# Kernel optimization log

Hardware: AMD Instinct MI355X
Metric: run time of the kernel (lower is better)

Reference implementation:

```python
import jax, jax.numpy as jnp
import numpy as np

B, T, D, N, H = 1, 256, 512, 8, 64  # batch, seq, d_model, n_heads, d_head
INIT_STD = 0.02
IGNORE = -1000000.0
DUMMY_LOGIT = -1000.0


def setup_inputs() -> dict:
    key = jax.random.key(0)
    ks = jax.random.split(key, 9)
    std = INIT_STD
    inp = {
        'normalized_resid_pre': jax.random.normal(ks[0], (B, T, D), dtype=jnp.float32),
        'W_K1': jax.random.normal(ks[1], (N, D, H), dtype=jnp.float32) * std,
        'W_K2': jax.random.normal(ks[2], (N, D, H), dtype=jnp.float32) * std,
        'W_Q':  jax.random.normal(ks[3], (N, D, H), dtype=jnp.float32) * std,
        'W_V1': jax.random.normal(ks[4], (N, D, H), dtype=jnp.float32) * std,
        'W_V2': jax.random.normal(ks[5], (N, D, H), dtype=jnp.float32) * std,
        'W_Kq': jax.random.normal(ks[6], (N, H, H, H), dtype=jnp.float32) * std,
        'W_Vq': jax.random.normal(ks[7], (N, H, H, H), dtype=jnp.float32) * std,
        'W_O':  jax.random.normal(ks[8], (N, H, D), dtype=jnp.float32) * std,
        'b_K1': jnp.zeros((N, H), dtype=jnp.float32),
        'b_K2': jnp.zeros((N, H), dtype=jnp.float32),
        'b_Q':  jnp.zeros((N, H), dtype=jnp.float32),
        'b_V1': jnp.zeros((N, H), dtype=jnp.float32),
        'b_V2': jnp.zeros((N, H), dtype=jnp.float32),
        'b_O':  jnp.zeros((D,), dtype=jnp.float32),
    }
    return inp


def _trittention(x, W_K1, W_K2, W_Q, W_V1, W_V2, W_Kq, W_Vq, W_O,
                 b_K1, b_K2, b_Q, b_V1, b_V2, b_O):
    b, t, d = x.shape
    n, _, h = W_Q.shape
    proj = lambda W, bias: jnp.einsum('ndh,bpd->bpnh', W, x) + bias
    k1 = proj(W_K1, b_K1)  # (b, t, n, h)
    k2 = proj(W_K2, b_K2)
    q  = proj(W_Q,  b_Q)
    v1 = proj(W_V1, b_V1)
    v2 = proj(W_V2, b_V2)

    # bilinear value over pairs of positions: (b, n, h, s, t) -> flatten (s t)
    v = jnp.einsum('bsni,btnj,nijh->bnhst', v1, v2, W_Vq)
    v = v.reshape(b, n, h, t * t)

    # cubic scores: (b, n, s, t, r) with s=k1 pos, t=k2 pos, r=query pos
    step1 = jnp.einsum('brnk,nijk->bnrij', q, W_Kq)
    step2 = jnp.einsum('bnrij,btnj->bnrit', step1, k2)
    attn = jnp.einsum('bnrit,bsni->bnstr', step2, k1)

    # causal + ordering mask (order_attn=True, attn_eq=False):
    # masked if s>=r or t>=r or s>=t
    s_idx = jnp.arange(t)[:, None, None]
    t_idx = jnp.arange(t)[None, :, None]
    r_idx = jnp.arange(t)[None, None, :]
    mask = (s_idx >= r_idx) | (t_idx >= r_idx) | (s_idx >= t_idx)
    attn = jnp.where(mask, IGNORE, attn)

    # rearrange 'b n s t r -> b n r (s t)' and scale by d_head
    attn = jnp.transpose(attn, (0, 1, 4, 2, 3)).reshape(b, n, t, t * t) / h

    # causal_attn=True: append dummy logit / zero value slot
    dummy_logit = jnp.full((b, n, t, 1), DUMMY_LOGIT, dtype=attn.dtype)
    attn = jnp.concatenate([attn, dummy_logit], axis=-1)
    dummy_value = jnp.zeros((b, n, h, 1), dtype=v.dtype)
    v = jnp.concatenate([v, dummy_value], axis=-1)

    attn = jax.nn.softmax(attn, axis=-1)
    z = jnp.einsum('bnql,bnhl->bqnh', attn, v)
    out = jnp.einsum('bpnh,nhd->bpd', z, W_O) + b_O  # sum over heads folded in
    return out


def reference(normalized_resid_pre, W_K1, W_K2, W_Q, W_V1, W_V2, W_Kq, W_Vq, W_O,
              b_K1, b_K2, b_Q, b_V1, b_V2, b_O):
    return _trittention(normalized_resid_pre, W_K1, W_K2, W_Q, W_V1, W_V2,
                        W_Kq, W_Vq, W_O, b_K1, b_K2, b_Q, b_V1, b_V2, b_O)
```

## Files before the change

kernel.cpp:

```cpp
#include <hip/hip_runtime.h>
#include <hip/hip_bf16.h>
#include <math.h>

#define TT 256
#define DD 512
#define NN 8
#define HH 64
#define PROJ 131072

typedef __attribute__((ext_vector_type(8))) short short8v;
typedef __attribute__((ext_vector_type(4))) short short4v;
typedef __attribute__((ext_vector_type(4))) float f32x4;

__device__ __forceinline__ short f2bf(float x) {
    union { float f; unsigned u; } v; v.f = x;
    unsigned r = (v.u + 0x7FFFu + ((v.u >> 16) & 1u)) >> 16;
    return (short)r;
}

#define LGKM0 asm volatile("s_waitcnt lgkmcnt(0)" ::: "memory")

#define F_NUM  0
#define F_DEN  131072
#define F_END  133120
#define S_PB   0
#define S_XB   655360
#define S_WB   786432
#define S_KQB  2097152
#define S_VQB  4194304
#define S_WOB  6291456
#define S_S1B  6553600
#define S_AB   14942208
#define S_GB   23330816

__global__ __launch_bounds__(256) void prep_kernel(
    const float* __restrict__ x, const float* __restrict__ W_Kq,
    const float* __restrict__ W0, const float* __restrict__ W1,
    const float* __restrict__ W2, const float* __restrict__ W3,
    const float* __restrict__ W4, const float* __restrict__ Vq,
    const float* __restrict__ WO, short* __restrict__ sb, float* __restrict__ fz)
{
    __shared__ float plds[64 * 129];
    int b = blockIdx.x;
    int tid = threadIdx.x;
    if (b < 1024) {
        int i = b * 256 + tid;
        const float4 f0 = *(const float4*)(W_Kq + (size_t)i * 8);
        const float4 f1 = *(const float4*)(W_Kq + (size_t)i * 8 + 4);
        short8v o;
        o[0]=f2bf(f0.x); o[1]=f2bf(f0.y); o[2]=f2bf(f0.z); o[3]=f2bf(f0.w);
        o[4]=f2bf(f1.x); o[5]=f2bf(f1.y); o[6]=f2bf(f1.z); o[7]=f2bf(f1.w);
        *(short8v*)(sb + S_KQB + (size_t)i * 8) = o;
    } else if (b < 1088) {
        int i = (b - 1024) * 256 + tid;
        const float4 f0 = *(const float4*)(x + (size_t)i * 8);
        const float4 f1 = *(const float4*)(x + (size_t)i * 8 + 4);
        short8v o;
        o[0]=f2bf(f0.x); o[1]=f2bf(f0.y); o[2]=f2bf(f0.z); o[3]=f2bf(f0.w);
        o[4]=f2bf(f1.x); o[5]=f2bf(f1.y); o[6]=f2bf(f1.z); o[7]=f2bf(f1.w);
        *(short8v*)(sb + S_XB + (size_t)i * 8) = o;
    } else if (b < 1128) {
        int pn = b - 1088; int p = pn >> 3, n = pn & 7;
        const float* Wp = (p==0)?W0:(p==1)?W1:(p==2)?W2:(p==3)?W3:W4;
        const float* src = Wp + (size_t)n * DD * HH;
        short* dst = sb + S_WB + (size_t)pn * HH * DD;
        for (int d0 = 0; d0 < DD; d0 += 64) {
            __syncthreads();
            for (int it = 0; it < 16; ++it) {
                int m = it * 256 + tid;
                int dl = m >> 6, h = m & 63;
                plds[h * 65 + dl] = src[(size_t)(d0 + dl) * 64 + h];
            }
            __syncthreads();
            int h = tid >> 2, seg = tid & 3;
            short8v o0, o1;
            #pragma unroll
            for (int e = 0; e < 8; ++e) o0[e] = f2bf(plds[h * 65 + seg * 16 + e]);
            #pragma unroll
            for (int e = 0; e < 8; ++e) o1[e] = f2bf(plds[h * 65 + seg * 16 + 8 + e]);
            *(short8v*)(dst + (size_t)h * DD + d0 + seg * 16) = o0;
            *(short8v*)(dst + (size_t)h * DD + d0 + seg * 16 + 8) = o1;
        }
    } else if (b < 1640) {
        int bb = b - 1128; int n = bb >> 6, i = bb & 63;
        const float* src = Vq + (size_t)(n * 64 + i) * 4096;
        for (int it = 0; it < 16; ++it) {
            int m = it * 256 + tid;
            int j = m >> 6, h = m & 63;
            plds[h * 65 + j] = src[(size_t)j * 64 + h];
        }
        __syncthreads();
        int h = tid >> 2, seg = tid & 3;
        short8v o0, o1;
        #pragma unroll
        for (int e = 0; e < 8; ++e) o0[e] = f2bf(plds[h * 65 + seg * 16 + e]);
        #pragma unroll
        for (int e = 0; e < 8; ++e) o1[e] = f2bf(plds[h * 65 + seg * 16 + 8 + e]);
        short* dst = sb + S_VQB + (size_t)n * 262144 + (size_t)h * 4096 + i * 64 + seg * 16;
        *(short8v*)dst = o0;
        *(short8v*)(dst + 8) = o1;
    } else if (b < 1672) {
        int bb = b - 1640; int dc = bb & 7, nhc = bb >> 3;
        for (int it = 0; it < 32; ++it) {
            int m = it * 256 + tid;
            int nhl = m >> 6, dl = m & 63;
            plds[dl * 129 + nhl] = WO[(size_t)(nhc * 128 + nhl) * 512 + dc * 64 + dl];
        }
        __syncthreads();
        for (int it = 0; it < 4; ++it) {
            int m = it * 256 + tid;
            int dl = m >> 4, seg = m & 15;
            short8v o;
            #pragma unroll
            for (int e = 0; e < 8; ++e) o[e] = f2bf(plds[dl * 129 + seg * 8 + e]);
            *(short8v*)(sb + S_WOB + (size_t)(dc * 64 + dl) * 512 + nhc * 128 + seg * 8) = o;
        }
    } else {
        int i = (b - 1672) * 1024 + tid * 4;
        *(float4*)(fz + i) = make_float4(0.f, 0.f, 0.f, 0.f);
    }
}

__global__ __launch_bounds__(512) void proj_kernel(
    const short* __restrict__ xb, const short* __restrict__ Wb,
    const float* __restrict__ bK1, const float* __restrict__ bK2,
    const float* __restrict__ bQ,  const float* __restrict__ bV1,
    const float* __restrict__ bV2, short* __restrict__ Pb) {
    int p = blockIdx.x, n = blockIdx.y, mhalf = blockIdx.z;
    int wv = threadIdx.x >> 6, lane = threadIdx.x & 63, g = lane >> 4, c = lane & 15;
    __shared__ short wlds[64 * 520];
    __shared__ short sbuf[8][16 * 72];
    const short* wsrc = Wb + (size_t)(p * 8 + n) * HH * DD;
    for (int it = 0; it < 8; ++it) {
        int idx = it * 512 + threadIdx.x;
        int h = idx >> 6, seg = idx & 63;
        *(short8v*)(&wlds[h * 520 + seg * 8]) = *(const short8v*)(wsrc + (size_t)h * DD + seg * 8);
    }
    __syncthreads();
    int mt = mhalf * 8 + wv;
    f32x4 acc[4];
    #pragma unroll
    for (int ct = 0; ct < 4; ++ct) acc[ct] = (f32x4){0.f, 0.f, 0.f, 0.f};
    for (int ks = 0; ks < 16; ++ks) {
        short8v a = *(const short8v*)(xb + (size_t)(mt * 16 + c) * DD + ks * 32 + g * 8);
        #pragma unroll
        for (int ct = 0; ct < 4; ++ct) {
            short8v b = *(const short8v*)(&wlds[(ct * 16 + c) * 520 + ks * 32 + g * 8]);
            acc[ct] = __builtin_amdgcn_mfma_f32_16x16x32_bf16(a, b, acc[ct], 0, 0, 0);
        }
    }
    const float* bp = (p == 0) ? bK1 : (p == 1) ? bK2 : (p == 2) ? bQ : (p == 3) ? bV1 : bV2;
    short* sbw = &sbuf[wv][0];
    #pragma unroll
    for (int ct = 0; ct < 4; ++ct) {
        float bias = bp[n * 64 + ct * 16 + c];
        #pragma unroll
        for (int m = 0; m < 4; ++m)
            sbw[(g * 4 + m) * 72 + ct * 16 + c] = f2bf(acc[ct][m] + bias);
    }
    LGKM0;
    int rl = lane & 15, sg = lane >> 4;
    short8v o0 = *(const short8v*)(&sbw[rl * 72 + sg * 16]);
    short8v o1 = *(const short8v*)(&sbw[rl * 72 + sg * 16 + 8]);
    short* dst = Pb + (size_t)p * PROJ + (size_t)(n * 256 + mt * 16 + rl) * 64 + sg * 16;
    *(short8v*)dst = o0;
    *(short8v*)(dst + 8) = o1;
}

__global__ __launch_bounds__(256) void bgemm_kernel(
    const short* __restrict__ A0, const short* __restrict__ B0, short* __restrict__ O0,
    const short* __restrict__ A1, const short* __restrict__ B1, short* __restrict__ O1) {
    int mt = blockIdx.x, n = blockIdx.y, z = blockIdx.z;
    const short* A = (z < 4) ? A0 : A1;
    const short* B = (z < 4) ? B0 : B1;
    short* out = (z < 4) ? O0 : O1;
    int cgq = z & 3;
    int wv = threadIdx.x >> 6, lane = threadIdx.x & 63, g = lane >> 4, c = lane & 15;
    __shared__ short sbuf[4][16 * 72];
    short* sbw = &sbuf[wv][0];
    const short* abase = A + ((size_t)n * 256 + mt * 16 + c) * 64 + g * 8;
    short8v a0 = *(const short8v*)abase;
    short8v a1 = *(const short8v*)(abase + 32);
    for (int cg = cgq * 16 + wv; cg < cgq * 16 + 16; cg += 4) {
        f32x4 acc[4];
        #pragma unroll
        for (int jt = 0; jt < 4; ++jt) acc[jt] = (f32x4){0.f, 0.f, 0.f, 0.f};
        const short* bb = B + ((size_t)n * 4096 + cg * 64) * 64;
        #pragma unroll
        for (int jt = 0; jt < 4; ++jt) {
            short8v b0 = *(const short8v*)(bb + (size_t)(jt * 16 + c) * 64 + g * 8);
            short8v b1 = *(const short8v*)(bb + (size_t)(jt * 16 + c) * 64 + g * 8 + 32);
            acc[jt] = __builtin_amdgcn_mfma_f32_16x16x32_bf16(a0, b0, acc[jt], 0, 0, 0);
            acc[jt] = __builtin_amdgcn_mfma_f32_16x16x32_bf16(a1, b1, acc[jt], 0, 0, 0);
        }
        LGKM0;
        #pragma unroll
        for (int jt = 0; jt < 4; ++jt)
            #pragma unroll
            for (int m = 0; m < 4; ++m)
                sbw[(g * 4 + m) * 72 + jt * 16 + c] = f2bf(acc[jt][m]);
        LGKM0;
        int rl = lane & 15, sg = lane >> 4;
        short8v o0 = *(const short8v*)(&sbw[rl * 72 + sg * 16]);
        short8v o1 = *(const short8v*)(&sbw[rl * 72 + sg * 16 + 8]);
        short* dst = out + ((size_t)n * 256 + mt * 16 + rl) * 4096 + cg * 64 + sg * 16;
        *(short8v*)dst = o0;
        *(short8v*)(dst + 8) = o1;
    }
}

__global__ __launch_bounds__(256) void gmat_kernel(const short* __restrict__ S1b,
                                                   const short* __restrict__ K2b,
                                                   short* __restrict__ G) {
    int bid = blockIdx.x;
    int n = bid & 7;
    int tt = (bid >> 3) & 15;
    int rq = bid >> 7;
    int wv = threadIdx.x >> 6, lane = threadIdx.x & 63, g = lane >> 4, c = lane & 15;
    int t0 = tt * 16;
    __shared__ short sbuf[4][16 * 68];
    short* sbw = &sbuf[wv][0];
    const short* abase = K2b + ((size_t)n * TT + t0 + c) * 64 + g * 8;
    short8v a0 = *(const short8v*)abase;
    short8v a1 = *(const short8v*)(abase + 32);
    for (int r = t0 + rq * 4 + wv; r < 256; r += 16) {
        const short* bb = S1b + ((size_t)(n * 256 + r) * 64) * 64;
        f32x4 acc[4];
        #pragma unroll
        for (int it = 0; it < 4; ++it) {
            short8v b0 = *(const short8v*)(bb + (size_t)(it * 16 + c) * 64 + g * 8);
            short8v b1 = *(const short8v*)(bb + (size_t)(it * 16 + c) * 64 + g * 8 + 32);
            acc[it] = (f32x4){0.f, 0.f, 0.f, 0.f};
            acc[it] = __builtin_amdgcn_mfma_f32_16x16x32_bf16(a0, b0, acc[it], 0, 0, 0);
            acc[it] = __builtin_amdgcn_mfma_f32_16x16x32_bf16(a1, b1, acc[it], 0, 0, 0);
        }
        LGKM0;
        #pragma unroll
        for (int it = 0; it < 4; ++it)
            #pragma unroll
            for (int m = 0; m < 4; ++m)
                sbw[(g * 4 + m) * 68 + it * 16 + c] = f2bf(acc[it][m]);
        LGKM0;
        int trow = lane >> 2, seg = (lane & 3) * 16;
        short8v o0 = *(const short8v*)(&sbw[trow * 68 + seg]);
        short8v o1 = *(const short8v*)(&sbw[trow * 68 + seg + 8]);
        short* dst = G + (((size_t)(n * TT + t0 + trow)) * TT + r) * 64 + seg;
        *(short8v*)dst = o0;
        *(short8v*)(dst + 8) = o1;
    }
}

__global__ __launch_bounds__(1024) void attn_kernel(
    const short* __restrict__ K1b, const short* __restrict__ V1b,
    const short* __restrict__ Gm, const short* __restrict__ Ab,
    float* __restrict__ num, float* __restrict__ den)
{
    int bid = blockIdx.x;
    int n = bid & 7;
    int rest = bid >> 3;
    int pair = rest >> 2;
    int sig = rest & 3;
    int tid = threadIdx.x;
    int wv = tid >> 6, lane = tid & 63, g = lane >> 4, c = lane & 15;

    __shared__ short k1lds[64 * 72];
    __shared__ short v1lds[64 * 72];
    __shared__ short u_lds[8][64][68];

    int t0H = (31 - pair) * 8;
    int stmaxK = (t0H + 6) >> 4;
    int cntK = (stmaxK >= sig) ? ((stmaxK - sig) >> 2) + 1 : 0;
    for (int idx = tid; idx < cntK * 128; idx += 1024) {
        int row = idx >> 3, seg = idx & 7;
        int s = (sig + (row >> 4) * 4) * 16 + (row & 15);
        *(short8v*)(&k1lds[row * 72 + seg * 8]) =
            *(const short8v*)(K1b + ((size_t)n * TT + s) * 64 + seg * 8);
        *(short8v*)(&v1lds[row * 72 + seg * 8]) =
            *(const short8v*)(V1b + ((size_t)n * TT + s) * 64 + seg * 8);
    }
    __syncthreads();

    f32x4 numacc[4];
    #pragma unroll
    for (int b = 0; b < 4; ++b) numacc[b] = (f32x4){0.f, 0.f, 0.f, 0.f};
    float denacc = 0.f;
    int rt = wv;
    int lU = wv >> 2, hU = wv & 3;

    const short* vr = &v1lds[(lU * 16 + c) * 72 + g * 8];
    short8v vf0 = *(const short8v*)vr;
    short8v vf1 = *(const short8v*)(vr + 32);

    for (int part = 0; part < 2; ++part) {
        int t0 = part ? t0H : pair * 8;

        __syncthreads();
        for (int tl = 0; tl < 8; ++tl) {
            int t = t0 + tl;
            int stm = (t - 1) >> 4;
            int cntU = (t >= 1 && stm >= sig) ? ((stm - sig) >> 2) + 1 : 0;
            if (lU >= cntU) continue;
            const short* ar = Ab + (size_t)(n * TT + t) * 4096 + (hU * 16 + c) * 64 + g * 8;
            short8v ab0 = *(const short8v*)ar;
            short8v ab1 = *(const short8v*)(ar + 32);
            f32x4 ucc = (f32x4){0.f, 0.f, 0.f, 0.f};
            ucc = __builtin_amdgcn_mfma_f32_16x16x32_bf16(vf0, ab0, ucc, 0, 0, 0);
            ucc = __builtin_amdgcn_mfma_f32_16x16x32_bf16(vf1, ab1, ucc, 0, 0, 0);
            short4v uo;
            #pragma unroll
            for (int m = 0; m < 4; ++m) uo[m] = f2bf(ucc[m]);
            *(short4v*)(&u_lds[tl][hU * 16 + c][lU * 16 + g * 4]) = uo;
        }
        __syncthreads();

        for (int tl = 0; tl < 8; ++tl) {
            int t = t0 + tl;
            if (t < 1 || t > 254) continue;
            int rt_start = (t + 1) >> 4;
            int stmaxU = (t - 1) >> 4;
            int cntU = (stmaxU >= sig) ? ((stmaxU - sig) >> 2) + 1 : 0;
            if (cntU == 0 || rt < rt_start) continue;

            const short* gb = Gm + (((size_t)(n * TT + t) * TT) + rt * 16 + c) * 64 + g * 8;
            short8v gf0 = *(const short8v*)gb;
            short8v gf1 = *(const short8v*)(gb + 32);
            int r = rt * 16 + c;

            for (int loc = 0; loc < cntU; ++loc) {
                int s_base = (sig + loc * 4) * 16;
                const short* kr = &k1lds[(loc * 16 + c) * 72 + g * 8];
                short8v af0 = *(const short8v*)kr;
                short8v af1 = *(const short8v*)(kr + 32);
                f32x4 lg = (f32x4){0.f, 0.f, 0.f, 0.f};
                lg = __builtin_amdgcn_mfma_f32_16x16x32_bf16(af0, gf0, lg, 0, 0, 0);
                lg = __builtin_amdgcn_mfma_f32_16x16x32_bf16(af1, gf1, lg, 0, 0, 0);
                short4v eb;
                float dsum = 0.f;
                #pragma unroll
                for (int m = 0; m < 4; ++m) {
                    int s = s_base + g * 4 + m;
                    float e = (s < t && r > t) ? __expf(lg[m] * 0.015625f) : 0.f;
                    dsum += e;
                    eb[m] = f2bf(e);
                }
                denacc += dsum;
                #pragma unroll
                for (int hs = 0; hs < 4; ++hs) {
                    short4v ub = *(const short4v*)(&u_lds[tl][hs * 16 + c][loc * 16 + g * 4]);
                    numacc[hs] = __builtin_amdgcn_mfma_f32_16x16x16bf16_1k(eb, ub, numacc[hs], 0, 0, 0);
                }
            }
        }
    }

    if (__any(denacc != 0.f)) {
        float v = denacc;
        v += __shfl_xor(v, 16);
        v += __shfl_xor(v, 32);
        if (lane < 16) atomicAdd(&den[n * TT + rt * 16 + lane], v);
        #pragma unroll
        for (int hs = 0; hs < 4; ++hs)
            #pragma unroll
            for (int m = 0; m < 4; ++m)
                atomicAdd(&num[((size_t)(n * TT + rt * 16 + g * 4 + m)) * 64 + hs * 16 + c],
                          numacc[hs][m]);
    }
}

__global__ __launch_bounds__(512) void out_kernel(const float* __restrict__ num,
                                                  const float* __restrict__ den,
                                                  const short* __restrict__ WOb,
                                                  const float* __restrict__ bO,
                                                  float* __restrict__ out) {
    int mt = blockIdx.x & 15, dq = blockIdx.x >> 4;
    int wv = threadIdx.x >> 6, lane = threadIdx.x & 63, g = lane >> 4, c = lane & 15;
    int dt0 = dq * 16 + wv * 2;
    int t = mt * 16 + c;
    f32x4 acc[2];
    acc[0] = (f32x4){0.f, 0.f, 0.f, 0.f};
    acc[1] = (f32x4){0.f, 0.f, 0.f, 0.f};
    for (int ks = 0; ks < 16; ++ks) {
        int nh = ks * 32 + g * 8;
        int nn = nh >> 6, h = nh & 63;
        float dv = den[nn * 256 + t];
        float rcp = (dv > 0.f) ? 1.f / dv : 0.f;
        const float* np = num + ((size_t)(nn * 256 + t) * 64 + h);
        float4 f0 = *(const float4*)np;
        float4 f1 = *(const float4*)(np + 4);
        short8v a;
        a[0]=f2bf(f0.x*rcp); a[1]=f2bf(f0.y*rcp); a[2]=f2bf(f0.z*rcp); a[3]=f2bf(f0.w*rcp);
        a[4]=f2bf(f1.x*rcp); a[5]=f2bf(f1.y*rcp); a[6]=f2bf(f1.z*rcp); a[7]=f2bf(f1.w*rcp);
        #pragma unroll
        for (int u = 0; u < 2; ++u) {
            short8v b = *(const short8v*)(WOb + (size_t)((dt0 + u) * 16 + c) * 512 + ks * 32 + g * 8);
            acc[u] = __builtin_amdgcn_mfma_f32_16x16x32_bf16(a, b, acc[u], 0, 0, 0);
        }
    }
    #pragma unroll
    for (int u = 0; u < 2; ++u) {
        int d = (dt0 + u) * 16 + c;
        float bias = bO[d];
        #pragma unroll
        for (int m = 0; m < 4; ++m)
            out[(size_t)(mt * 16 + g * 4 + m) * 512 + d] = acc[u][m] + bias;
    }
}

extern "C" void kernel_launch(void* const* d_in, const int* in_sizes, int n_in,
                              void* d_out, int out_size, void* d_ws, size_t ws_size,
                              hipStream_t stream) {
    const float* x    = (const float*)d_in[0];
    const float* W_K1 = (const float*)d_in[1];
    const float* W_K2 = (const float*)d_in[2];
    const float* W_Q  = (const float*)d_in[3];
    const float* W_V1 = (const float*)d_in[4];
    const float* W_V2 = (const float*)d_in[5];
    const float* W_Kq = (const float*)d_in[6];
    const float* W_Vq = (const float*)d_in[7];
    const float* W_O  = (const float*)d_in[8];
    const float* b_K1 = (const float*)d_in[9];
    const float* b_K2 = (const float*)d_in[10];
    const float* b_Q  = (const float*)d_in[11];
    const float* b_V1 = (const float*)d_in[12];
    const float* b_V2 = (const float*)d_in[13];
    const float* b_O  = (const float*)d_in[14];
    float* ws = (float*)d_ws;
    short* sb = (short*)(ws + F_END);
    float* out = (float*)d_out;

    prep_kernel<<<1802, 256, 0, stream>>>(x, W_Kq, W_K1, W_K2, W_Q, W_V1, W_V2,
                                          W_Vq, W_O, sb, ws + F_NUM);

    proj_kernel<<<dim3(5, 8, 2), 512, 0, stream>>>(sb + S_XB, sb + S_WB,
                                                   b_K1, b_K2, b_Q, b_V1, b_V2, sb + S_PB);

    bgemm_kernel<<<dim3(16, 8, 8), 256, 0, stream>>>(
        sb + S_PB + 2 * PROJ, sb + S_KQB, sb + S_S1B,
        sb + S_PB + 4 * PROJ, sb + S_VQB, sb + S_AB);

    gmat_kernel<<<512, 256, 0, stream>>>(sb + S_S1B, sb + S_PB + 1 * PROJ, sb + S_GB);

    attn_kernel<<<512, 1024, 0, stream>>>(sb + S_PB, sb + S_PB + 3 * PROJ,
                                          sb + S_GB, sb + S_AB,
                                          ws + F_NUM, ws + F_DEN);

    out_kernel<<<32, 512, 0, stream>>>(ws + F_NUM, ws + F_DEN, sb + S_WOB, b_O, out);
}
```

Measured before the change: 152.3 us.

## Re-split attention work into smaller blocks with double-buffered U tiles

Attention work is re-partitioned. Blocks shrink from 1024 to 512 threads and each covers one 8-position t-chunk and one half of the query row tiles, replacing the old pairing of a low and a high t-chunk; the grid grows from 512 to 1536 blocks. The per-t U tile is now computed inline into a two-slot LDS buffer with one barrier per t instead of an 8-slot staging pass, which cuts LDS use so more blocks fit per CU. Blocks with no work exit early. The trade-offs are recomputing the K1/V1 loads and U per half-split, plus possible load imbalance because the old triangular pairing is gone.

```diff
diff --git a/kernel.cpp b/kernel.cpp
--- a/kernel.cpp
+++ b/kernel.cpp
@@ -250,27 +250,31 @@
     }
 }
 
-__global__ __launch_bounds__(1024) void attn_kernel(
+__global__ __launch_bounds__(512, 8) void attn_kernel(
     const short* __restrict__ K1b, const short* __restrict__ V1b,
     const short* __restrict__ Gm, const short* __restrict__ Ab,
     float* __restrict__ num, float* __restrict__ den)
 {
     int bid = blockIdx.x;
     int n = bid & 7;
-    int rest = bid >> 3;
-    int pair = rest >> 2;
-    int sig = rest & 3;
+    int sig = (bid >> 3) & 3;
+    int q = bid >> 5;
+    int tc, rthalf;
+    if (q < 32) { tc = q >> 1; rthalf = q & 1; }
+    else        { tc = q - 16; rthalf = 1; }
     int tid = threadIdx.x;
     int wv = tid >> 6, lane = tid & 63, g = lane >> 4, c = lane & 15;
 
+    int t0 = tc * 8;
+    int stmaxK = (t0 + 6) >> 4;
+    int cntK = (stmaxK >= sig) ? ((stmaxK - sig) >> 2) + 1 : 0;
+    if (cntK == 0) return;
+
     __shared__ short k1lds[64 * 72];
     __shared__ short v1lds[64 * 72];
-    __shared__ short u_lds[8][64][68];
-
-    int t0H = (31 - pair) * 8;
-    int stmaxK = (t0H + 6) >> 4;
-    int cntK = (stmaxK >= sig) ? ((stmaxK - sig) >> 2) + 1 : 0;
-    for (int idx = tid; idx < cntK * 128; idx += 1024) {
+    __shared__ short u_lds[2][64][68];
+
+    for (int idx = tid; idx < cntK * 128; idx += 512) {
         int row = idx >> 3, seg = idx & 7;
         int s = (sig + (row >> 4) * 4) * 16 + (row & 15);
         *(short8v*)(&k1lds[row * 72 + seg * 8]) =
@@ -280,47 +284,59 @@
     }
     __syncthreads();
 
+    int hU = wv & 3, locA = wv >> 2, locB = locA + 2;
+    int rt = rthalf * 8 + wv;
+    int rtmax = rthalf * 8 + 7;
+
     f32x4 numacc[4];
     #pragma unroll
     for (int b = 0; b < 4; ++b) numacc[b] = (f32x4){0.f, 0.f, 0.f, 0.f};
     float denacc = 0.f;
-    int rt = wv;
-    int lU = wv >> 2, hU = wv & 3;
-
-    const short* vr = &v1lds[(lU * 16 + c) * 72 + g * 8];
-    short8v vf0 = *(const short8v*)vr;
-    short8v vf1 = *(const short8v*)(vr + 32);
-
-    for (int part = 0; part < 2; ++part) {
-        int t0 = part ? t0H : pair * 8;
-
-        __syncthreads();
-        for (int tl = 0; tl < 8; ++tl) {
-            int t = t0 + tl;
-            int stm = (t - 1) >> 4;
-            int cntU = (t >= 1 && stm >= sig) ? ((stm - sig) >> 2) + 1 : 0;
-            if (lU >= cntU) continue;
+    int ub = 0;
+
+    for (int tl = 0; tl < 8; ++tl) {
+        int t = t0 + tl;
+        if (t < 1 || t > 254) continue;
+        int stmaxU = (t - 1) >> 4;
+        int cntU = (stmaxU >= sig) ? ((stmaxU - sig) >> 2) + 1 : 0;
+        if (cntU == 0) continue;
+        int rt_start = (t + 1) >> 4;
+        if (rt_start > rtmax) continue;
+
+        short (*uw)[68] = u_lds[ub]; ub ^= 1;
+        int nT = cntU * 4;
+        if (wv < nT) {
             const short* ar = Ab + (size_t)(n * TT + t) * 4096 + (hU * 16 + c) * 64 + g * 8;
             short8v ab0 = *(const short8v*)ar;
             short8v ab1 = *(const short8v*)(ar + 32);
-            f32x4 ucc = (f32x4){0.f, 0.f, 0.f, 0.f};
-            ucc = __builtin_amdgcn_mfma_f32_16x16x32_bf16(vf0, ab0, ucc, 0, 0, 0);
-            ucc = __builtin_amdgcn_mfma_f32_16x16x32_bf16(vf1, ab1, ucc, 0, 0, 0);
-            short4v uo;
-            #pragma unroll
-            for (int m = 0; m < 4; ++m) uo[m] = f2bf(ucc[m]);
-            *(short4v*)(&u_lds[tl][hU * 16 + c][lU * 16 + g * 4]) = uo;
+            {
+                const short* vr = &v1lds[(locA * 16 + c) * 72 + g * 8];
+                short8v vf0 = *(const short8v*)vr;
+                short8v vf1 = *(const short8v*)(vr + 32);
+                f32x4 u = (f32x4){0.f, 0.f, 0.f, 0.f};
+                u = __builtin_amdgcn_mfma_f32_16x16x32_bf16(vf0, ab0, u, 0, 0, 0);
+                u = __builtin_amdgcn_mfma_f32_16x16x32_bf16(vf1, ab1, u, 0, 0, 0);
+                short4v uo;
+                #pragma unroll
+                for (int m = 0; m < 4; ++m) uo[m] = f2bf(u[m]);
+                *(short4v*)(&uw[hU * 16 + c][locA * 16 + g * 4]) = uo;
+            }
+            if (wv + 8 < nT) {
+                const short* vr = &v1lds[(locB * 16 + c) * 72 + g * 8];
+                short8v vf0 = *(const short8v*)vr;
+                short8v vf1 = *(const short8v*)(vr + 32);
+                f32x4 u = (f32x4){0.f, 0.f, 0.f, 0.f};
+                u = __builtin_amdgcn_mfma_f32_16x16x32_bf16(vf0, ab0, u, 0, 0, 0);
+                u = __builtin_amdgcn_mfma_f32_16x16x32_bf16(vf1, ab1, u, 0, 0, 0);
+                short4v uo;
+                #pragma unroll
+                for (int m = 0; m < 4; ++m) uo[m] = f2bf(u[m]);
+                *(short4v*)(&uw[hU * 16 + c][locB * 16 + g * 4]) = uo;
+            }
         }
         __syncthreads();
 
-        for (int tl = 0; tl < 8; ++tl) {
-            int t = t0 + tl;
-            if (t < 1 || t > 254) continue;
-            int rt_start = (t + 1) >> 4;
-            int stmaxU = (t - 1) >> 4;
-            int cntU = (stmaxU >= sig) ? ((stmaxU - sig) >> 2) + 1 : 0;
-            if (cntU == 0 || rt < rt_start) continue;
-
+        if (rt >= rt_start) {
             const short* gb = Gm + (((size_t)(n * TT + t) * TT) + rt * 16 + c) * 64 + g * 8;
             short8v gf0 = *(const short8v*)gb;
             short8v gf1 = *(const short8v*)(gb + 32);
@@ -346,8 +362,8 @@
                 denacc += dsum;
                 #pragma unroll
                 for (int hs = 0; hs < 4; ++hs) {
-                    short4v ub = *(const short4v*)(&u_lds[tl][hs * 16 + c][loc * 16 + g * 4]);
-                    numacc[hs] = __builtin_amdgcn_mfma_f32_16x16x16bf16_1k(eb, ub, numacc[hs], 0, 0, 0);
+                    short4v ubf = *(const short4v*)(&uw[hs * 16 + c][loc * 16 + g * 4]);
+                    numacc[hs] = __builtin_amdgcn_mfma_f32_16x16x16bf16_1k(eb, ubf, numacc[hs], 0, 0, 0);
                 }
             }
         }
@@ -440,7 +456,7 @@
 
     gmat_kernel<<<512, 256, 0, stream>>>(sb + S_S1B, sb + S_PB + 1 * PROJ, sb + S_GB);
 
-    attn_kernel<<<512, 1024, 0, stream>>>(sb + S_PB, sb + S_PB + 3 * PROJ,
+    attn_kernel<<<1536, 512, 0, stream>>>(sb + S_PB, sb + S_PB + 3 * PROJ,
                                           sb + S_GB, sb + S_AB,
                                           ws + F_NUM, ws + F_DEN);
 
```

Result: no change. 151.1 us (-0.8%).

## Reassociate trilinear scores via K2·W_Kq and drop the G-matrix kernel

Applied to the files above, without the earlier changes.

The cubic score contraction is reassociated. bgemm now multiplies K2 by a transposed W_Kq to build a per-t matrix M. attn_kernel computes Y = M·q on the fly per query tile, then contracts it with K1, instead of reading a precomputed G tensor of size (t, r, i) from memory. This removes the gmat_kernel and its large global write and read. It also regrids attn_kernel into 768 blocks of 512 threads over (t chunk, r half), with per-t U tiles built in shared memory. The cost is extra MFMA work to recompute Y per t, and the new work split may be less balanced.

```diff
diff --git a/kernel.cpp b/kernel.cpp
--- a/kernel.cpp
+++ b/kernel.cpp
@@ -29,9 +29,8 @@
 #define S_KQB  2097152
 #define S_VQB  4194304
 #define S_WOB  6291456
-#define S_S1B  6553600
+#define S_MB   6553600
 #define S_AB   14942208
-#define S_GB   23330816
 
 __global__ __launch_bounds__(256) void prep_kernel(
     const float* __restrict__ x, const float* __restrict__ W_Kq,
@@ -43,24 +42,34 @@
     __shared__ float plds[64 * 129];
     int b = blockIdx.x;
     int tid = threadIdx.x;
-    if (b < 1024) {
-        int i = b * 256 + tid;
-        const float4 f0 = *(const float4*)(W_Kq + (size_t)i * 8);
-        const float4 f1 = *(const float4*)(W_Kq + (size_t)i * 8 + 4);
-        short8v o;
-        o[0]=f2bf(f0.x); o[1]=f2bf(f0.y); o[2]=f2bf(f0.z); o[3]=f2bf(f0.w);
-        o[4]=f2bf(f1.x); o[5]=f2bf(f1.y); o[6]=f2bf(f1.z); o[7]=f2bf(f1.w);
-        *(short8v*)(sb + S_KQB + (size_t)i * 8) = o;
-    } else if (b < 1088) {
-        int i = (b - 1024) * 256 + tid;
+    if (b < 512) {
+        int n = b >> 6, i = b & 63;
+        const float* src = W_Kq + (size_t)(n * 64 + i) * 4096;
+        for (int it = 0; it < 16; ++it) {
+            int m = it * 256 + tid;
+            int j = m >> 6, k = m & 63;
+            plds[k * 65 + j] = src[m];
+        }
+        __syncthreads();
+        int k = tid >> 2, seg = tid & 3;
+        short8v o0, o1;
+        #pragma unroll
+        for (int e = 0; e < 8; ++e) o0[e] = f2bf(plds[k * 65 + seg * 16 + e]);
+        #pragma unroll
+        for (int e = 0; e < 8; ++e) o1[e] = f2bf(plds[k * 65 + seg * 16 + 8 + e]);
+        short* dst = sb + S_KQB + (size_t)n * 262144 + (size_t)(i * 64 + k) * 64 + seg * 16;
+        *(short8v*)dst = o0;
+        *(short8v*)(dst + 8) = o1;
+    } else if (b < 576) {
+        int i = (b - 512) * 256 + tid;
         const float4 f0 = *(const float4*)(x + (size_t)i * 8);
         const float4 f1 = *(const float4*)(x + (size_t)i * 8 + 4);
         short8v o;
         o[0]=f2bf(f0.x); o[1]=f2bf(f0.y); o[2]=f2bf(f0.z); o[3]=f2bf(f0.w);
         o[4]=f2bf(f1.x); o[5]=f2bf(f1.y); o[6]=f2bf(f1.z); o[7]=f2bf(f1.w);
         *(short8v*)(sb + S_XB + (size_t)i * 8) = o;
-    } else if (b < 1128) {
-        int pn = b - 1088; int p = pn >> 3, n = pn & 7;
+    } else if (b < 616) {
+        int pn = b - 576; int p = pn >> 3, n = pn & 7;
         const float* Wp = (p==0)?W0:(p==1)?W1:(p==2)?W2:(p==3)?W3:W4;
         const float* src = Wp + (size_t)n * DD * HH;
         short* dst = sb + S_WB + (size_t)pn * HH * DD;
@@ -81,8 +90,8 @@
             *(short8v*)(dst + (size_t)h * DD + d0 + seg * 16) = o0;
             *(short8v*)(dst + (size_t)h * DD + d0 + seg * 16 + 8) = o1;
         }
-    } else if (b < 1640) {
-        int bb = b - 1128; int n = bb >> 6, i = bb & 63;
+    } else if (b < 1128) {
+        int bb = b - 616; int n = bb >> 6, i = bb & 63;
         const float* src = Vq + (size_t)(n * 64 + i) * 4096;
         for (int it = 0; it < 16; ++it) {
             int m = it * 256 + tid;
@@ -99,8 +108,8 @@
         short* dst = sb + S_VQB + (size_t)n * 262144 + (size_t)h * 4096 + i * 64 + seg * 16;
         *(short8v*)dst = o0;
         *(short8v*)(dst + 8) = o1;
-    } else if (b < 1672) {
-        int bb = b - 1640; int dc = bb & 7, nhc = bb >> 3;
+    } else if (b < 1160) {
+        int bb = b - 1128; int dc = bb & 7, nhc = bb >> 3;
         for (int it = 0; it < 32; ++it) {
             int m = it * 256 + tid;
             int nhl = m >> 6, dl = m & 63;
@@ -116,7 +125,7 @@
             *(short8v*)(sb + S_WOB + (size_t)(dc * 64 + dl) * 512 + nhc * 128 + seg * 8) = o;
         }
     } else {
-        int i = (b - 1672) * 1024 + tid * 4;
+        int i = (b - 1160) * 1024 + tid * 4;
         *(float4*)(fz + i) = make_float4(0.f, 0.f, 0.f, 0.f);
     }
 }
@@ -209,146 +218,104 @@
     }
 }
 
-__global__ __launch_bounds__(256) void gmat_kernel(const short* __restrict__ S1b,
-                                                   const short* __restrict__ K2b,
-                                                   short* __restrict__ G) {
-    int bid = blockIdx.x;
-    int n = bid & 7;
-    int tt = (bid >> 3) & 15;
-    int rq = bid >> 7;
-    int wv = threadIdx.x >> 6, lane = threadIdx.x & 63, g = lane >> 4, c = lane & 15;
-    int t0 = tt * 16;
-    __shared__ short sbuf[4][16 * 68];
-    short* sbw = &sbuf[wv][0];
-    const short* abase = K2b + ((size_t)n * TT + t0 + c) * 64 + g * 8;
-    short8v a0 = *(const short8v*)abase;
-    short8v a1 = *(const short8v*)(abase + 32);
-    for (int r = t0 + rq * 4 + wv; r < 256; r += 16) {
-        const short* bb = S1b + ((size_t)(n * 256 + r) * 64) * 64;
-        f32x4 acc[4];
-        #pragma unroll
-        for (int it = 0; it < 4; ++it) {
-            short8v b0 = *(const short8v*)(bb + (size_t)(it * 16 + c) * 64 + g * 8);
-            short8v b1 = *(const short8v*)(bb + (size_t)(it * 16 + c) * 64 + g * 8 + 32);
-            acc[it] = (f32x4){0.f, 0.f, 0.f, 0.f};
-            acc[it] = __builtin_amdgcn_mfma_f32_16x16x32_bf16(a0, b0, acc[it], 0, 0, 0);
-            acc[it] = __builtin_amdgcn_mfma_f32_16x16x32_bf16(a1, b1, acc[it], 0, 0, 0);
-        }
-        LGKM0;
-        #pragma unroll
-        for (int it = 0; it < 4; ++it)
-            #pragma unroll
-            for (int m = 0; m < 4; ++m)
-                sbw[(g * 4 + m) * 68 + it * 16 + c] = f2bf(acc[it][m]);
-        LGKM0;
-        int trow = lane >> 2, seg = (lane & 3) * 16;
-        short8v o0 = *(const short8v*)(&sbw[trow * 68 + seg]);
-        short8v o1 = *(const short8v*)(&sbw[trow * 68 + seg + 8]);
-        short* dst = G + (((size_t)(n * TT + t0 + trow)) * TT + r) * 64 + seg;
-        *(short8v*)dst = o0;
-        *(short8v*)(dst + 8) = o1;
-    }
-}
-
-__global__ __launch_bounds__(1024) void attn_kernel(
+__global__ __launch_bounds__(512, 6) void attn_kernel(
     const short* __restrict__ K1b, const short* __restrict__ V1b,
-    const short* __restrict__ Gm, const short* __restrict__ Ab,
+    const short* __restrict__ Qb,  const short* __restrict__ Mb,
+    const short* __restrict__ Ab,
     float* __restrict__ num, float* __restrict__ den)
 {
     int bid = blockIdx.x;
     int n = bid & 7;
-    int rest = bid >> 3;
-    int pair = rest >> 2;
-    int sig = rest & 3;
+    int z = bid >> 3;
+    int tc4, rthalf;
+    if (z < 64) { tc4 = z >> 1; rthalf = z & 1; }
+    else        { tc4 = z - 32; rthalf = 1; }
     int tid = threadIdx.x;
     int wv = tid >> 6, lane = tid & 63, g = lane >> 4, c = lane & 15;
-
-    __shared__ short k1lds[64 * 72];
-    __shared__ short v1lds[64 * 72];
-    __shared__ short u_lds[8][64][68];
-
-    int t0H = (31 - pair) * 8;
-    int stmaxK = (t0H + 6) >> 4;
-    int cntK = (stmaxK >= sig) ? ((stmaxK - sig) >> 2) + 1 : 0;
-    for (int idx = tid; idx < cntK * 128; idx += 1024) {
-        int row = idx >> 3, seg = idx & 7;
-        int s = (sig + (row >> 4) * 4) * 16 + (row & 15);
-        *(short8v*)(&k1lds[row * 72 + seg * 8]) =
-            *(const short8v*)(K1b + ((size_t)n * TT + s) * 64 + seg * 8);
-        *(short8v*)(&v1lds[row * 72 + seg * 8]) =
-            *(const short8v*)(V1b + ((size_t)n * TT + s) * 64 + seg * 8);
-    }
-    __syncthreads();
+    int rt = rthalf * 8 + wv;
+    int t0 = tc4 * 4;
+
+    __shared__ short u_lds[64 * 260];
+    __shared__ short mlds[64 * 72];
+
+    const short* qrow = Qb + ((size_t)(n * 256) + rt * 16 + c) * 64 + g * 8;
+    short8v qf0 = *(const short8v*)qrow;
+    short8v qf1 = *(const short8v*)(qrow + 32);
 
     f32x4 numacc[4];
     #pragma unroll
     for (int b = 0; b < 4; ++b) numacc[b] = (f32x4){0.f, 0.f, 0.f, 0.f};
     float denacc = 0.f;
-    int rt = wv;
-    int lU = wv >> 2, hU = wv & 3;
-
-    const short* vr = &v1lds[(lU * 16 + c) * 72 + g * 8];
-    short8v vf0 = *(const short8v*)vr;
-    short8v vf1 = *(const short8v*)(vr + 32);
-
-    for (int part = 0; part < 2; ++part) {
-        int t0 = part ? t0H : pair * 8;
+
+    for (int tl = 0; tl < 4; ++tl) {
+        int t = t0 + tl;
+        int cntU = (t >= 1 && t <= 254) ? (((t - 1) >> 4) + 1) : 0;
 
         __syncthreads();
-        for (int tl = 0; tl < 8; ++tl) {
-            int t = t0 + tl;
-            int stm = (t - 1) >> 4;
-            int cntU = (t >= 1 && stm >= sig) ? ((stm - sig) >> 2) + 1 : 0;
-            if (lU >= cntU) continue;
-            const short* ar = Ab + (size_t)(n * TT + t) * 4096 + (hU * 16 + c) * 64 + g * 8;
-            short8v ab0 = *(const short8v*)ar;
-            short8v ab1 = *(const short8v*)(ar + 32);
-            f32x4 ucc = (f32x4){0.f, 0.f, 0.f, 0.f};
-            ucc = __builtin_amdgcn_mfma_f32_16x16x32_bf16(vf0, ab0, ucc, 0, 0, 0);
-            ucc = __builtin_amdgcn_mfma_f32_16x16x32_bf16(vf1, ab1, ucc, 0, 0, 0);
-            short4v uo;
-            #pragma unroll
-            for (int m = 0; m < 4; ++m) uo[m] = f2bf(ucc[m]);
-            *(short4v*)(&u_lds[tl][hU * 16 + c][lU * 16 + g * 4]) = uo;
+        if (cntU) {
+            {
+                int row = tid >> 3, seg = tid & 7;
+                *(short8v*)(&mlds[row * 72 + seg * 8]) =
+                    *(const short8v*)(Mb + ((size_t)(n * 256 + t)) * 4096 + row * 64 + seg * 8);
+            }
+            for (int task = wv; task < cntU * 4; task += 8) {
+                int loc = task >> 2, hs = task & 3;
+                const short* vr = V1b + ((size_t)(n * 256) + loc * 16 + c) * 64 + g * 8;
+                short8v vf0 = *(const short8v*)vr;
+                short8v vf1 = *(const short8v*)(vr + 32);
+                const short* ar = Ab + ((size_t)(n * 256 + t)) * 4096 + (hs * 16 + c) * 64 + g * 8;
+                short8v ab0 = *(const short8v*)ar;
+                short8v ab1 = *(const short8v*)(ar + 32);
+                f32x4 u = (f32x4){0.f, 0.f, 0.f, 0.f};
+                u = __builtin_amdgcn_mfma_f32_16x16x32_bf16(vf0, ab0, u, 0, 0, 0);
+                u = __builtin_amdgcn_mfma_f32_16x16x32_bf16(vf1, ab1, u, 0, 0, 0);
+                short4v uo;
+                #pragma unroll
+                for (int m = 0; m < 4; ++m) uo[m] = f2bf(u[m]);
+                *(short4v*)(&u_lds[(hs * 16 + c) * 260 + loc * 16 + g * 4]) = uo;
+            }
         }
         __syncthreads();
-
-        for (int tl = 0; tl < 8; ++tl) {
-            int t = t0 + tl;
-            if (t < 1 || t > 254) continue;
-            int rt_start = (t + 1) >> 4;
-            int stmaxU = (t - 1) >> 4;
-            int cntU = (stmaxU >= sig) ? ((stmaxU - sig) >> 2) + 1 : 0;
-            if (cntU == 0 || rt < rt_start) continue;
-
-            const short* gb = Gm + (((size_t)(n * TT + t) * TT) + rt * 16 + c) * 64 + g * 8;
-            short8v gf0 = *(const short8v*)gb;
-            short8v gf1 = *(const short8v*)(gb + 32);
-            int r = rt * 16 + c;
-
-            for (int loc = 0; loc < cntU; ++loc) {
-                int s_base = (sig + loc * 4) * 16;
-                const short* kr = &k1lds[(loc * 16 + c) * 72 + g * 8];
-                short8v af0 = *(const short8v*)kr;
-                short8v af1 = *(const short8v*)(kr + 32);
-                f32x4 lg = (f32x4){0.f, 0.f, 0.f, 0.f};
-                lg = __builtin_amdgcn_mfma_f32_16x16x32_bf16(af0, gf0, lg, 0, 0, 0);
-                lg = __builtin_amdgcn_mfma_f32_16x16x32_bf16(af1, gf1, lg, 0, 0, 0);
-                short4v eb;
-                float dsum = 0.f;
-                #pragma unroll
-                for (int m = 0; m < 4; ++m) {
-                    int s = s_base + g * 4 + m;
-                    float e = (s < t && r > t) ? __expf(lg[m] * 0.015625f) : 0.f;
-                    dsum += e;
-                    eb[m] = f2bf(e);
-                }
-                denacc += dsum;
-                #pragma unroll
-                for (int hs = 0; hs < 4; ++hs) {
-                    short4v ub = *(const short4v*)(&u_lds[tl][hs * 16 + c][loc * 16 + g * 4]);
-                    numacc[hs] = __builtin_amdgcn_mfma_f32_16x16x16bf16_1k(eb, ub, numacc[hs], 0, 0, 0);
-                }
+        if (!cntU) continue;
+        int rt_start = (t + 1) >> 4;
+        if (rt < rt_start) continue;
+
+        short4v yb[4];
+        #pragma unroll
+        for (int it = 0; it < 4; ++it) {
+            short8v mf0 = *(const short8v*)(&mlds[(it * 16 + c) * 72 + g * 8]);
+            short8v mf1 = *(const short8v*)(&mlds[(it * 16 + c) * 72 + 32 + g * 8]);
+            f32x4 y = (f32x4){0.f, 0.f, 0.f, 0.f};
+            y = __builtin_amdgcn_mfma_f32_16x16x32_bf16(mf0, qf0, y, 0, 0, 0);
+            y = __builtin_amdgcn_mfma_f32_16x16x32_bf16(mf1, qf1, y, 0, 0, 0);
+            #pragma unroll
+            for (int m = 0; m < 4; ++m) yb[it][m] = f2bf(y[m]);
+        }
+
+        int r = rt * 16 + c;
+        const short* krow = K1b + ((size_t)(n * 256) + c) * 64 + g * 4;
+        for (int loc = 0; loc < cntU; ++loc) {
+            const short* kr = krow + (size_t)(loc * 16) * 64;
+            f32x4 lg = (f32x4){0.f, 0.f, 0.f, 0.f};
+            #pragma unroll
+            for (int it = 0; it < 4; ++it) {
+                short4v ka = *(const short4v*)(kr + it * 16);
+                lg = __builtin_amdgcn_mfma_f32_16x16x16bf16_1k(ka, yb[it], lg, 0, 0, 0);
+            }
+            short4v eb;
+            float dsum = 0.f;
+            #pragma unroll
+            for (int m = 0; m < 4; ++m) {
+                int s = loc * 16 + g * 4 + m;
+                float e = (s < t && r > t) ? __expf(lg[m] * 0.015625f) : 0.f;
+                dsum += e;
+                eb[m] = f2bf(e);
+            }
+            denacc += dsum;
+            #pragma unroll
+            for (int hs = 0; hs < 4; ++hs) {
+                short4v ub = *(const short4v*)(&u_lds[(hs * 16 + c) * 260 + loc * 16 + g * 4]);
+                numacc[hs] = __builtin_amdgcn_mfma_f32_16x16x16bf16_1k(eb, ub, numacc[hs], 0, 0, 0);
             }
         }
     }
@@ -428,21 +395,19 @@
     short* sb = (short*)(ws + F_END);
     float* out = (float*)d_out;
 
-    prep_kernel<<<1802, 256, 0, stream>>>(x, W_Kq, W_K1, W_K2, W_Q, W_V1, W_V2,
+    prep_kernel<<<1290, 256, 0, stream>>>(x, W_Kq, W_K1, W_K2, W_Q, W_V1, W_V2,
                                           W_Vq, W_O, sb, ws + F_NUM);
 
     proj_kernel<<<dim3(5, 8, 2), 512, 0, stream>>>(sb + S_XB, sb + S_WB,
                                                    b_K1, b_K2, b_Q, b_V1, b_V2, sb + S_PB);
 
     bgemm_kernel<<<dim3(16, 8, 8), 256, 0, stream>>>(
-        sb + S_PB + 2 * PROJ, sb + S_KQB, sb + S_S1B,
+        sb + S_PB + 1 * PROJ, sb + S_KQB, sb + S_MB,
         sb + S_PB + 4 * PROJ, sb + S_VQB, sb + S_AB);
 
-    gmat_kernel<<<512, 256, 0, stream>>>(sb + S_S1B, sb + S_PB + 1 * PROJ, sb + S_GB);
-
-    attn_kernel<<<512, 1024, 0, stream>>>(sb + S_PB, sb + S_PB + 3 * PROJ,
-                                          sb + S_GB, sb + S_AB,
-                                          ws + F_NUM, ws + F_DEN);
+    attn_kernel<<<768, 512, 0, stream>>>(sb + S_PB, sb + S_PB + 3 * PROJ,
+                                         sb + S_PB + 2 * PROJ, sb + S_MB, sb + S_AB,
+                                         ws + F_NUM, ws + F_DEN);
 
     out_kernel<<<32, 512, 0, stream>>>(ws + F_NUM, ws + F_DEN, sb + S_WOB, b_O, out);
 }
```

New measurement: 177.8 us. +16.7%, slower.
